# Kernel optimization log

Measured on AMD Instinct MI355X. Metric: run time of the kernel, lower is better.

## Reference

```python
import jax, jax.numpy as jnp
import numpy as np

T = 4.0  # distillation temperature (init kwarg)
B, C = 64, 1000


def _hierarchical_softmax(x, targets):
    # x, targets: [B, C]
    xd = jax.lax.stop_gradient(x)
    # t2[b,i,k] = relu(x[b,i] - stop_grad(x[b,k]))  -> [B, C, C]
    t2 = jnp.maximum(x[:, :, None] - xd[:, None, :], 0.0)
    # t3[b,i] = mean_k targets[b,k] * t2[b,i,k]
    t3 = (targets[:, None, :] * t2).mean(axis=-1)  # [B, C]
    choice = targets * jnp.exp(-t3) + (1.0 - targets)
    ex = jnp.exp(x)
    neg_sum = ((1.0 - targets) * ex).sum(axis=-1, keepdims=True)  # [B, 1]
    return ex / (choice * neg_sum + ex)


def setup_inputs() -> dict:
    key = jax.random.key(0)
    k1, k2, k3 = jax.random.split(key, 3)
    y_s = jax.random.normal(k1, (B, C), dtype=jnp.float32)
    y_t = jax.random.normal(k2, (B, C), dtype=jnp.float32)
    w = jax.random.randint(k3, (B, C), 0, 2).astype(jnp.float32)  # multi-hot targets
    return {"y_s": y_s, "y_t": y_t, "w": w}


def reference(y_s, y_t, w):
    # 'w' branch of DistillKL.forward (dead code: preds/thr/sigmoid/max_min omitted)
    p_s = _hierarchical_softmax(y_s / 4.0, w)
    p_t = _hierarchical_softmax(y_t / 4.0, w)
    p_s_1 = jnp.minimum(p_s, 1.0)  # clamp(max=1)
    p_t_1 = jnp.minimum(p_t, 1.0)
    # abs(...) >= 0 so clamp(min=0,max=1) == min(.,1)
    pos_expo = w * jnp.minimum(jnp.abs((p_t_1 + 1.0) / 2.0 - p_s_1), 1.0) ** 0.25
    neg_expo = (1.0 - w) * jnp.minimum(jnp.abs(p_t_1 / 2.0 - p_s_1), 1.0)
    expt = pos_expo + neg_expo
    ps = jnp.maximum(p_s_1 ** expt, 1e-7)
    pt = jnp.maximum(p_t, 1e-7)
    # my_kl: -(target * log(pred)).sum(dim=1).mean() * T**2
    return -(pt * jnp.log(ps)).sum(axis=1).mean() * (T * T)
```

## Files before the change

kernel.cpp:

```cpp
#include <hip/hip_runtime.h>


#define BN 64
#define CN 1000
#define SPLITS 8
#define CHUNK 125
#define THREADS 128
#define NEG_LOG_EPS -16.118095650958319f

__global__ __launch_bounds__(THREADS) void distill_part(
    const float* __restrict__ ys, const float* __restrict__ yt,
    const float* __restrict__ w, float* __restrict__ part)
{
    const int b = blockIdx.x;
    const int s = blockIdx.y;
    const int tid = threadIdx.x;
    const int lane = tid & 63;
    const int wid = tid >> 6;

    __shared__ float xs[CN], xt[CN];
    __shared__ float xsm[CN], xtm[CN];
    __shared__ float wsh[CN];
    __shared__ float redns[4];
    __shared__ float redterm[2];

    const float* ysr = ys + b * CN;
    const float* ytr = yt + b * CN;
    const float* wr  = w  + b * CN;

    float ns_s = 0.f, ns_t = 0.f;
    for (int k = tid; k < CN; k += THREADS) {
        float a  = ysr[k] * 0.25f;
        float c2 = ytr[k] * 0.25f;
        float wk = wr[k];
        xs[k] = a; xt[k] = c2; wsh[k] = wk;
        bool pos = (wk != 0.f);
        xsm[k] = pos ? a  : 1e30f;
        xtm[k] = pos ? c2 : 1e30f;
        float nw = 1.f - wk;
        ns_s += nw * expf(a);
        ns_t += nw * expf(c2);
    }
    #pragma unroll
    for (int off = 32; off > 0; off >>= 1) {
        ns_s += __shfl_down(ns_s, off);
        ns_t += __shfl_down(ns_t, off);
    }
    if (lane == 0) { redns[wid * 2] = ns_s; redns[wid * 2 + 1] = ns_t; }
    __syncthreads();
    const float negsum_s = redns[0] + redns[2];
    const float negsum_t = redns[1] + redns[3];

    float term = 0.f;
    const int i = s * CHUNK + tid;
    if (tid < CHUNK && i < CN) {
        const float xsi = xs[i], xti = xt[i];
        float acc_s = 0.f, acc_t = 0.f;
        #pragma unroll 4
        for (int k = 0; k < CN; ++k) {
            acc_s += fmaxf(xsi - xsm[k], 0.f);
            acc_t += fmaxf(xti - xtm[k], 0.f);
        }
        const float t3s = acc_s * (1.0f / CN);
        const float t3t = acc_t * (1.0f / CN);
        const float wi = wsh[i];
        const float ch_s = wi * expf(-t3s) + (1.f - wi);
        const float ch_t = wi * expf(-t3t) + (1.f - wi);
        const float exs = expf(xsi), ext = expf(xti);
        const float p_s = exs / (ch_s * negsum_s + exs);
        const float p_t = ext / (ch_t * negsum_t + ext);
        const float ps1 = fminf(p_s, 1.f);
        const float pt1 = fminf(p_t, 1.f);
        const float vpos = fminf(fabsf((pt1 + 1.f) * 0.5f - ps1), 1.f);
        const float vneg = fminf(fabsf(pt1 * 0.5f - ps1), 1.f);
        const float expt = wi * sqrtf(sqrtf(vpos)) + (1.f - wi) * vneg;
        const float logps = fmaxf(expt * logf(ps1), NEG_LOG_EPS);
        term = fmaxf(p_t, 1e-7f) * logps;
    }
    #pragma unroll
    for (int off = 32; off > 0; off >>= 1) term += __shfl_down(term, off);
    __syncthreads();
    if (lane == 0) redterm[wid] = term;
    __syncthreads();
    if (tid == 0) part[b * SPLITS + s] = redterm[0] + redterm[1];
}

__global__ __launch_bounds__(64) void distill_final(
    const float* __restrict__ part, float* __restrict__ out)
{
    const int t = threadIdx.x;
    float v = 0.f;
    for (int j = t; j < BN * SPLITS; j += 64) v += part[j];
    #pragma unroll
    for (int off = 32; off > 0; off >>= 1) v += __shfl_down(v, off);
    if (t == 0) out[0] = -0.25f * v;
}

extern "C" void kernel_launch(void* const* d_in, const int* in_sizes, int n_in,
                              void* d_out, int out_size, void* d_ws, size_t ws_size,
                              hipStream_t stream) {
    const float* ys = (const float*)d_in[0];
    const float* yt = (const float*)d_in[1];
    const float* w  = (const float*)d_in[2];
    float* out  = (float*)d_out;
    float* part = (float*)d_ws;

    dim3 grid(BN, SPLITS);
    distill_part<<<grid, THREADS, 0, stream>>>(ys, yt, w, part);
    distill_final<<<1, 64, 0, stream>>>(part, out);
}
```

Baseline: 84.68 us.

## Split pairwise k-loop across four thread groups with float4 LDS reads

Increases the block to 512 threads and splits the O(C) inner pairwise relu-sum over k into four quarter ranges. Each 128-thread group accumulates a partial sum, and the partials are combined through shared memory. Arrays are padded to 1024 with sentinel values so each group can use float4 shared-memory loads and two accumulators per stream. The goal is to cut the serial per-thread loop length and raise occupancy and latency hiding. The cost is an extra reduction step, a sync, and some idle lanes.

```diff
diff --git a/kernel.cpp b/kernel.cpp
--- a/kernel.cpp
+++ b/kernel.cpp
@@ -3,9 +3,11 @@
 
 #define BN 64
 #define CN 1000
+#define CPAD 1024
 #define SPLITS 8
 #define CHUNK 125
-#define THREADS 128
+#define THREADS 512
+#define KQ (CPAD / 4)
 #define NEG_LOG_EPS -16.118095650958319f
 
 __global__ __launch_bounds__(THREADS) void distill_part(
@@ -17,11 +19,14 @@
     const int tid = threadIdx.x;
     const int lane = tid & 63;
     const int wid = tid >> 6;
+    const int l = tid & 127;
+    const int q = tid >> 7;
 
-    __shared__ float xs[CN], xt[CN];
-    __shared__ float xsm[CN], xtm[CN];
-    __shared__ float wsh[CN];
-    __shared__ float redns[4];
+    __shared__ __align__(16) float xs[CPAD], xt[CPAD];
+    __shared__ __align__(16) float xsm[CPAD], xtm[CPAD];
+    __shared__ float wsh[CPAD];
+    __shared__ float ps_s[THREADS], ps_t[THREADS];
+    __shared__ float redns[16];
     __shared__ float redterm[2];
 
     const float* ysr = ys + b * CN;
@@ -29,17 +34,23 @@
     const float* wr  = w  + b * CN;
 
     float ns_s = 0.f, ns_t = 0.f;
-    for (int k = tid; k < CN; k += THREADS) {
-        float a  = ysr[k] * 0.25f;
-        float c2 = ytr[k] * 0.25f;
-        float wk = wr[k];
-        xs[k] = a; xt[k] = c2; wsh[k] = wk;
-        bool pos = (wk != 0.f);
-        xsm[k] = pos ? a  : 1e30f;
-        xtm[k] = pos ? c2 : 1e30f;
-        float nw = 1.f - wk;
-        ns_s += nw * expf(a);
-        ns_t += nw * expf(c2);
+    #pragma unroll
+    for (int k = tid; k < CPAD; k += THREADS) {
+        if (k < CN) {
+            float a  = ysr[k] * 0.25f;
+            float c2 = ytr[k] * 0.25f;
+            float wk = wr[k];
+            xs[k] = a; xt[k] = c2; wsh[k] = wk;
+            bool pos = (wk != 0.f);
+            xsm[k] = pos ? a  : 1e30f;
+            xtm[k] = pos ? c2 : 1e30f;
+            float nw = 1.f - wk;
+            ns_s += nw * expf(a);
+            ns_t += nw * expf(c2);
+        } else {
+            xs[k] = 0.f; xt[k] = 0.f; wsh[k] = 0.f;
+            xsm[k] = 1e30f; xtm[k] = 1e30f;
+        }
     }
     #pragma unroll
     for (int off = 32; off > 0; off >>= 1) {
@@ -48,19 +59,39 @@
     }
     if (lane == 0) { redns[wid * 2] = ns_s; redns[wid * 2 + 1] = ns_t; }
     __syncthreads();
-    const float negsum_s = redns[0] + redns[2];
-    const float negsum_t = redns[1] + redns[3];
+    float negsum_s = 0.f, negsum_t = 0.f;
+    #pragma unroll
+    for (int u = 0; u < 8; ++u) {
+        negsum_s += redns[u * 2];
+        negsum_t += redns[u * 2 + 1];
+    }
+
+    const int i = s * CHUNK + l;
+    const float xsi = xs[i], xti = xt[i];
+    const float4* xsm4 = reinterpret_cast<const float4*>(xsm) + q * (KQ / 4);
+    const float4* xtm4 = reinterpret_cast<const float4*>(xtm) + q * (KQ / 4);
+    float as0 = 0.f, as1 = 0.f, at0 = 0.f, at1 = 0.f;
+    #pragma unroll 4
+    for (int j = 0; j < KQ / 4; ++j) {
+        float4 vs = xsm4[j];
+        float4 vt = xtm4[j];
+        as0 += fmaxf(xsi - vs.x, 0.f);
+        as1 += fmaxf(xsi - vs.y, 0.f);
+        as0 += fmaxf(xsi - vs.z, 0.f);
+        as1 += fmaxf(xsi - vs.w, 0.f);
+        at0 += fmaxf(xti - vt.x, 0.f);
+        at1 += fmaxf(xti - vt.y, 0.f);
+        at0 += fmaxf(xti - vt.z, 0.f);
+        at1 += fmaxf(xti - vt.w, 0.f);
+    }
+    ps_s[tid] = as0 + as1;
+    ps_t[tid] = at0 + at1;
+    __syncthreads();
 
     float term = 0.f;
-    const int i = s * CHUNK + tid;
-    if (tid < CHUNK && i < CN) {
-        const float xsi = xs[i], xti = xt[i];
-        float acc_s = 0.f, acc_t = 0.f;
-        #pragma unroll 4
-        for (int k = 0; k < CN; ++k) {
-            acc_s += fmaxf(xsi - xsm[k], 0.f);
-            acc_t += fmaxf(xti - xtm[k], 0.f);
-        }
+    if (tid < CHUNK) {
+        const float acc_s = ps_s[tid] + ps_s[tid + 128] + ps_s[tid + 256] + ps_s[tid + 384];
+        const float acc_t = ps_t[tid] + ps_t[tid + 128] + ps_t[tid + 256] + ps_t[tid + 384];
         const float t3s = acc_s * (1.0f / CN);
         const float t3t = acc_t * (1.0f / CN);
         const float wi = wsh[i];
@@ -79,8 +110,7 @@
     }
     #pragma unroll
     for (int off = 32; off > 0; off >>= 1) term += __shfl_down(term, off);
-    __syncthreads();
-    if (lane == 0) redterm[wid] = term;
+    if (wid < 2 && lane == 0) redterm[wid] = term;
     __syncthreads();
     if (tid == 0) part[b * SPLITS + s] = redterm[0] + redterm[1];
 }
```

Measured after the change: 71.97 us. -15.0%, faster.
